# Kernel tuning notes

Hardware: AMD Instinct MI355X
Metric: run time of the kernel (lower is better)

## Reference

```python
import jax, jax.numpy as jnp
import numpy as np

N_NODES = 50000
N_EDGES = 800000
N_GRAPHS = 128


def gcn_conv(x, row, col, W, b, num_nodes):
    # GCNConv: x' = D^-1/2 (A + I) D^-1/2 (x W) + b, with self-loops added.
    h = x @ W  # [N, out]
    # append self-loops
    sl = jnp.arange(num_nodes, dtype=row.dtype)
    r = jnp.concatenate([row, sl])
    c = jnp.concatenate([col, sl])
    deg = jax.ops.segment_sum(jnp.ones_like(r, dtype=h.dtype), r, num_segments=num_nodes)
    dinv = jnp.where(deg > 0, jax.lax.rsqrt(deg), 0.0)
    norm = dinv[r] * dinv[c]  # [E+N]
    msg = h[c] * norm[:, None]  # gather + scale
    out = jax.ops.segment_sum(msg, r, num_segments=num_nodes)
    return out + b


def setup_inputs() -> dict:
    key = jax.random.key(0)
    k = jax.random.split(key, 6)
    x = jax.random.normal(k[0], (N_NODES, 256), dtype=jnp.float32)
    edge_index = jax.random.randint(k[1], (2, N_EDGES), 0, N_NODES, dtype=jnp.int32)
    batch = jnp.sort(jax.random.randint(k[2], (N_NODES,), 0, N_GRAPHS, dtype=jnp.int32))
    W1 = jax.random.normal(k[3], (256, 128), dtype=jnp.float32) * (1.0 / np.sqrt(256))
    b1 = jnp.zeros((128,), dtype=jnp.float32)
    W2 = jax.random.normal(k[4], (128, 32), dtype=jnp.float32) * (1.0 / np.sqrt(128))
    b2 = jnp.zeros((32,), dtype=jnp.float32)
    return {"x": x, "edge_index": edge_index, "batch": batch,
            "W1": W1, "b1": b1, "W2": W2, "b2": b2}


def reference(x, edge_index, batch, W1, b1, W2, b2):
    row, col = edge_index[0], edge_index[1]
    h = gcn_conv(x, row, col, W1, b1, N_NODES)
    h = jax.nn.relu(h)
    # dropout is identity in eval mode (training=False)
    h = gcn_conv(h, row, col, W2, b2, N_NODES)
    # global_mean_pool over batch ids
    sums = jax.ops.segment_sum(h, batch, num_segments=N_GRAPHS)
    cnts = jax.ops.segment_sum(jnp.ones((N_NODES,), dtype=h.dtype), batch, num_segments=N_GRAPHS)
    pooled = sums / jnp.clip(cnts, 1.0)[:, None]  # [G, num_classes]
    return jax.nn.log_softmax(pooled, axis=1)
```

## Files before the change

kernel.cpp:

```cpp
#include <hip/hip_runtime.h>
#include <math.h>

#define N_NODES 50000
#define N_EDGES 800000
#define N_GRAPHS 128
#define DIM0 256
#define DIM1 128
#define DIM2 32

#define NBUCK 196
#define NEB 98

using f32x4 = __attribute__((ext_vector_type(4))) float;
using s16x8 = __attribute__((ext_vector_type(8))) short;

__device__ inline unsigned bf16pack(float a, float b) {
    unsigned ua = __float_as_uint(a), ub = __float_as_uint(b);
    ua = (ua + 0x7fffu + ((ua >> 16) & 1u)) >> 16;
    ub = (ub + 0x7fffu + ((ub >> 16) & 1u)) >> 16;
    return ua | (ub << 16);
}
__device__ inline float2 bf16x2(unsigned p) {
    return make_float2(__uint_as_float(p << 16), __uint_as_float(p & 0xffff0000u));
}

__device__ inline int featOf(int p) {
    return 32 * (p >> 5) + ((p >> 1) & 15) + 16 * (p & 1);
}

__global__ __launch_bounds__(256) void k_preph(const float* __restrict__ W1, uint* __restrict__ W1b,
                                               const float* __restrict__ W2, uint* __restrict__ W2b,
                                               const int* __restrict__ batch, int* gstart,
                                               const int* __restrict__ row, int* __restrict__ hist) {
    __shared__ int h[NBUCK];
    int b = blockIdx.x, t = threadIdx.x;
    if (b < NEB) {
        if (t < NBUCK) h[t] = 0;
        __syncthreads();
#pragma unroll
        for (int i = 0; i < 8; ++i) {
            int idx = b * 2048 + i * 256 + t;
            if (idx < N_EDGES / 4) {
                int4 r4 = ((const int4*)row)[idx];
                atomicAdd(&h[r4.x >> 8], 1);
                atomicAdd(&h[r4.y >> 8], 1);
                atomicAdd(&h[r4.z >> 8], 1);
                atomicAdd(&h[r4.w >> 8], 1);
            }
        }
        __syncthreads();
        if (t < NBUCK) hist[b * NBUCK + t] = h[t];
    } else {
        int g = (b - NEB) * 256 + t;
        {
            int s = g >> 9, tt = (g >> 6) & 7, q = (g >> 4) & 3, n = g & 15;
            int k0 = s * 32 + q * 8;
            int col = tt * 16 + n;
            uint4 o;
            o.x = bf16pack(W1[(size_t)(k0 + 0) * DIM1 + col], W1[(size_t)(k0 + 1) * DIM1 + col]);
            o.y = bf16pack(W1[(size_t)(k0 + 2) * DIM1 + col], W1[(size_t)(k0 + 3) * DIM1 + col]);
            o.z = bf16pack(W1[(size_t)(k0 + 4) * DIM1 + col], W1[(size_t)(k0 + 5) * DIM1 + col]);
            o.w = bf16pack(W1[(size_t)(k0 + 6) * DIM1 + col], W1[(size_t)(k0 + 7) * DIM1 + col]);
            ((uint4*)W1b)[g] = o;
        }
        if (g < 512) {
            int s = g >> 7, tt = (g >> 6) & 1, l = g & 63;
            int n = tt * 16 + (l & 15);
            int kb = s * 32 + (l >> 4) * 8;
            uint4 o;
            o.x = bf16pack(W2[(size_t)featOf(kb + 0) * DIM2 + n], W2[(size_t)featOf(kb + 1) * DIM2 + n]);
            o.y = bf16pack(W2[(size_t)featOf(kb + 2) * DIM2 + n], W2[(size_t)featOf(kb + 3) * DIM2 + n]);
            o.z = bf16pack(W2[(size_t)featOf(kb + 4) * DIM2 + n], W2[(size_t)featOf(kb + 5) * DIM2 + n]);
            o.w = bf16pack(W2[(size_t)featOf(kb + 6) * DIM2 + n], W2[(size_t)featOf(kb + 7) * DIM2 + n]);
            ((uint4*)W2b)[g] = o;
        }
        if (g <= N_GRAPHS) {
            int lo = 0, hi = N_NODES;
            while (lo < hi) { int mid = (lo + hi) >> 1; if (batch[mid] < g) lo = mid + 1; else hi = mid; }
            gstart[g] = lo;
        }
    }
}

__global__ __launch_bounds__(256) void k_place(const int* __restrict__ row, const int* __restrict__ col,
                                               const int* __restrict__ hist, uint* __restrict__ bb,
                                               int* __restrict__ bbase, int* __restrict__ btot) {
    __shared__ int cur[NBUCK];
    __shared__ int tot[NBUCK];
    __shared__ int sc[256];
    int blk = blockIdx.x, t = threadIdx.x;
    int pre = 0, to = 0;
    for (int b2 = 0; b2 < NEB; ++b2) {
        int v = (t < NBUCK) ? hist[b2 * NBUCK + t] : 0;
        to += v;
        if (b2 < blk) pre += v;
    }
    if (t < NBUCK) tot[t] = to;
    sc[t] = (t < NBUCK) ? to : 0;
    __syncthreads();
    for (int off = 1; off < 256; off <<= 1) {
        int x = (t >= off) ? sc[t - off] : 0;
        __syncthreads();
        sc[t] += x;
        __syncthreads();
    }
    if (t < NBUCK) {
        int base = sc[t] - tot[t];
        cur[t] = base + pre;
        if (blk == 0) { bbase[t] = base; btot[t] = tot[t]; }
    }
    __syncthreads();
#pragma unroll
    for (int i = 0; i < 8; ++i) {
        int idx = blk * 2048 + i * 256 + t;
        if (idx < N_EDGES / 4) {
            int4 r4 = ((const int4*)row)[idx];
            int4 c4 = ((const int4*)col)[idx];
            int rs[4] = {r4.x, r4.y, r4.z, r4.w};
            int cs[4] = {c4.x, c4.y, c4.z, c4.w};
#pragma unroll
            for (int j = 0; j < 4; ++j) {
                int pos = atomicAdd(&cur[rs[j] >> 8], 1);
                bb[pos] = ((uint)(rs[j] & 255) << 16) | (uint)cs[j];
            }
        }
    }
}

__global__ __launch_bounds__(256) void k_build(const int* __restrict__ bbase, const int* __restrict__ btot,
                                               const uint* __restrict__ bb,
                                               int* __restrict__ offs, int* __restrict__ cnt,
                                               ushort* __restrict__ csr) {
    __shared__ int c256[256];
    __shared__ int cur256[256];
    __shared__ int wsum[4];
    int b = blockIdx.x, t = threadIdx.x;
    int start = bbase[b];
    int n = btot[b];
    c256[t] = 0;
    __syncthreads();
    for (int i = t; i < n; i += 256) atomicAdd(&c256[bb[start + i] >> 16], 1);
    __syncthreads();
    int w = t >> 6, l = t & 63;
    int v = c256[t];
    int incl = v;
#pragma unroll
    for (int off = 1; off < 64; off <<= 1) {
        int x = __shfl_up(incl, off, 64);
        if (l >= off) incl += x;
    }
    if (l == 63) wsum[w] = incl;
    __syncthreads();
    int woff = 0;
    for (int i = 0; i < w; ++i) woff += wsum[i];
    int excl = incl - v + woff;
    cur256[t] = excl;
    int r = b * 256 + t;
    if (r < N_NODES) { offs[r] = start + excl; cnt[r] = v; }
    __syncthreads();
    for (int i = t; i < n; i += 256) {
        uint e = bb[start + i];
        int pos = atomicAdd(&cur256[e >> 16], 1);
        csr[start + pos] = (ushort)(e & 0xFFFFu);
    }
}

#define G1_BM 128
#define AS_LD 20
__global__ __launch_bounds__(256) void k_gemm1(const float* __restrict__ X, const uint* __restrict__ W1b,
                                               const int* __restrict__ cnt, unsigned* __restrict__ h1u) {
    __shared__ uint w1s[16384];
    __shared__ uint As[G1_BM * AS_LD];
    int t = threadIdx.x;
    int w = t >> 6, lane = t & 63, q = lane >> 4, m16 = lane & 15;
    int rowBase = blockIdx.x * G1_BM;

    {
        const uint4* src = (const uint4*)W1b;
        uint4* dst = (uint4*)w1s;
#pragma unroll
        for (int i = 0; i < 16; ++i) dst[i * 256 + t] = src[i * 256 + t];
    }

    f32x4 acc[2][8];
#pragma unroll
    for (int i = 0; i < 2; ++i)
#pragma unroll
        for (int j = 0; j < 8; ++j) acc[i][j] = (f32x4){0.f, 0.f, 0.f, 0.f};

    int ar = t >> 1, ah = t & 1;
    for (int s = 0; s < 8; ++s) {
        float4 f0 = {0,0,0,0}, f1 = {0,0,0,0}, f2 = {0,0,0,0}, f3 = {0,0,0,0};
        int grow = rowBase + ar;
        if (grow < N_NODES) {
            const float* src = X + (size_t)grow * DIM0 + s * 32 + ah * 16;
            f0 = *(const float4*)(src + 0);
            f1 = *(const float4*)(src + 4);
            f2 = *(const float4*)(src + 8);
            f3 = *(const float4*)(src + 12);
        }
        uint4 p0, p1;
        p0.x = bf16pack(f0.x, f0.y); p0.y = bf16pack(f0.z, f0.w);
        p0.z = bf16pack(f1.x, f1.y); p0.w = bf16pack(f1.z, f1.w);
        p1.x = bf16pack(f2.x, f2.y); p1.y = bf16pack(f2.z, f2.w);
        p1.z = bf16pack(f3.x, f3.y); p1.w = bf16pack(f3.z, f3.w);
        __syncthreads();
        *(uint4*)&As[ar * AS_LD + ah * 8 + 0] = p0;
        *(uint4*)&As[ar * AS_LD + ah * 8 + 4] = p1;
        __syncthreads();

        s16x8 af[2];
#pragma unroll
        for (int rt = 0; rt < 2; ++rt) {
            int arow = w * 32 + rt * 16 + m16;
            af[rt] = *(s16x8*)&As[arow * AS_LD + q * 4];
        }
#pragma unroll
        for (int tt = 0; tt < 8; ++tt) {
            s16x8 bf = *(s16x8*)&w1s[((s * 8 + tt) * 64 + lane) * 4];
            acc[0][tt] = __builtin_amdgcn_mfma_f32_16x16x32_bf16(af[0], bf, acc[0][tt], 0, 0, 0);
            acc[1][tt] = __builtin_amdgcn_mfma_f32_16x16x32_bf16(af[1], bf, acc[1][tt], 0, 0, 0);
        }
    }

#pragma unroll
    for (int rt = 0; rt < 2; ++rt) {
#pragma unroll
        for (int reg = 0; reg < 4; ++reg) {
            int row = rowBase + w * 32 + rt * 16 + q * 4 + reg;
            if (row < N_NODES) {
                float dv = rsqrtf((float)(cnt[row] + 1));
                unsigned* hr = h1u + (size_t)row * 64;
#pragma unroll
                for (int u = 0; u < 4; ++u)
                    hr[u * 16 + m16] = bf16pack(acc[rt][2 * u][reg] * dv, acc[rt][2 * u + 1][reg] * dv);
            }
        }
    }
}

#define A1_LD 68
__global__ __launch_bounds__(256) void k_agg1g2(const unsigned* __restrict__ h1u, const int* __restrict__ cnt,
                                                const int* __restrict__ offs, const ushort* __restrict__ csr,
                                                const float* __restrict__ b1, const uint* __restrict__ W2b,
                                                unsigned* __restrict__ h2u) {
    __shared__ uint a1tile[16 * A1_LD];
    __shared__ float sdi[16];
    int t = threadIdx.x;
    int wv = t >> 6, lane = t & 63;
    int nb16 = blockIdx.x * 16;

#pragma unroll
    for (int i = 0; i < 4; ++i) {
        int m = wv * 4 + i;
        int node = nb16 + m;
        float2 acc = bf16x2(h1u[(size_t)node * 64 + lane]);
        int n = cnt[node];
        const ushort* cp = csr + offs[node];
        int ec = 0;
        if (lane < n) ec = cp[lane];
        int j = 0;
        for (; j + 8 <= n; j += 8) {
            int c0 = __shfl(ec, j),     c1 = __shfl(ec, j + 1), c2 = __shfl(ec, j + 2), c3 = __shfl(ec, j + 3);
            int c4 = __shfl(ec, j + 4), c5 = __shfl(ec, j + 5), c6 = __shfl(ec, j + 6), c7 = __shfl(ec, j + 7);
            unsigned p0 = h1u[(size_t)c0 * 64 + lane];
            unsigned p1 = h1u[(size_t)c1 * 64 + lane];
            unsigned p2 = h1u[(size_t)c2 * 64 + lane];
            unsigned p3 = h1u[(size_t)c3 * 64 + lane];
            unsigned p4 = h1u[(size_t)c4 * 64 + lane];
            unsigned p5 = h1u[(size_t)c5 * 64 + lane];
            unsigned p6 = h1u[(size_t)c6 * 64 + lane];
            unsigned p7 = h1u[(size_t)c7 * 64 + lane];
            float2 v0 = bf16x2(p0), v1 = bf16x2(p1), v2 = bf16x2(p2), v3 = bf16x2(p3);
            float2 v4 = bf16x2(p4), v5 = bf16x2(p5), v6 = bf16x2(p6), v7 = bf16x2(p7);
            acc.x += (v0.x + v1.x) + (v2.x + v3.x) + (v4.x + v5.x) + (v6.x + v7.x);
            acc.y += (v0.y + v1.y) + (v2.y + v3.y) + (v4.y + v5.y) + (v6.y + v7.y);
        }
        for (; j + 4 <= n; j += 4) {
            int c0 = __shfl(ec, j), c1 = __shfl(ec, j + 1), c2 = __shfl(ec, j + 2), c3 = __shfl(ec, j + 3);
            unsigned p0 = h1u[(size_t)c0 * 64 + lane];
            unsigned p1 = h1u[(size_t)c1 * 64 + lane];
            unsigned p2 = h1u[(size_t)c2 * 64 + lane];
            unsigned p3 = h1u[(size_t)c3 * 64 + lane];
            float2 v0 = bf16x2(p0), v1 = bf16x2(p1), v2 = bf16x2(p2), v3 = bf16x2(p3);
            acc.x += (v0.x + v1.x) + (v2.x + v3.x);
            acc.y += (v0.y + v1.y) + (v2.y + v3.y);
        }
        for (; j < n; ++j) {
            int c = __shfl(ec, j);
            float2 v = bf16x2(h1u[(size_t)c * 64 + lane]);
            acc.x += v.x; acc.y += v.y;
        }
        float di = rsqrtf((float)(n + 1));
        if (lane == 0) sdi[m] = di;
        int f0 = (lane >> 4) * 32 + (lane & 15);
        acc.x = fmaxf(acc.x * di + b1[f0], 0.f);
        acc.y = fmaxf(acc.y * di + b1[f0 + 16], 0.f);
        a1tile[m * A1_LD + lane] = bf16pack(acc.x, acc.y);
    }
    __syncthreads();

    if (wv == 0) {
        int q = lane >> 4, m16 = lane & 15;
        f32x4 accA = (f32x4){0.f, 0.f, 0.f, 0.f};
        f32x4 accB = (f32x4){0.f, 0.f, 0.f, 0.f};
#pragma unroll
        for (int s = 0; s < 4; ++s) {
            s16x8 af = *(s16x8*)&a1tile[m16 * A1_LD + s * 16 + q * 4];
            s16x8 bf0 = *(const s16x8*)(W2b + (size_t)((s * 2 + 0) * 64 + lane) * 4);
            s16x8 bf1 = *(const s16x8*)(W2b + (size_t)((s * 2 + 1) * 64 + lane) * 4);
            accA = __builtin_amdgcn_mfma_f32_16x16x32_bf16(af, bf0, accA, 0, 0, 0);
            accB = __builtin_amdgcn_mfma_f32_16x16x32_bf16(af, bf1, accB, 0, 0, 0);
        }
#pragma unroll
        for (int r = 0; r < 4; ++r) {
            int node = nb16 + q * 4 + r;
            float dv = sdi[q * 4 + r];
            h2u[(size_t)node * 16 + m16] = bf16pack(accA[r] * dv, accB[r] * dv);
        }
    }
}

__global__ __launch_bounds__(256) void k_agg2(const unsigned* __restrict__ h2u, const int* __restrict__ cnt,
                                              const int* __restrict__ offs, const ushort* __restrict__ csr,
                                              const float* __restrict__ b2, float* __restrict__ a2) {
    int t = threadIdx.x;
    int node = blockIdx.x * 16 + (t >> 4);
    int l = t & 15;
    float2 acc = bf16x2(h2u[(size_t)node * 16 + l]);
    int n = cnt[node];
    const ushort* cp = csr + offs[node];
    for (int base = 0; base < n; base += 16) {
        int m = min(16, n - base);
        int ec = 0;
        if (l < m) ec = cp[base + l];
        int j = 0;
        for (; j + 4 <= m; j += 4) {
            int c0 = __shfl(ec, j, 16), c1 = __shfl(ec, j + 1, 16);
            int c2 = __shfl(ec, j + 2, 16), c3 = __shfl(ec, j + 3, 16);
            unsigned p0 = h2u[(size_t)c0 * 16 + l];
            unsigned p1 = h2u[(size_t)c1 * 16 + l];
            unsigned p2 = h2u[(size_t)c2 * 16 + l];
            unsigned p3 = h2u[(size_t)c3 * 16 + l];
            float2 v0 = bf16x2(p0), v1 = bf16x2(p1), v2 = bf16x2(p2), v3 = bf16x2(p3);
            acc.x += v0.x + v1.x + v2.x + v3.x;
            acc.y += v0.y + v1.y + v2.y + v3.y;
        }
        for (; j < m; ++j) {
            int c = __shfl(ec, j, 16);
            float2 v = bf16x2(h2u[(size_t)c * 16 + l]);
            acc.x += v.x; acc.y += v.y;
        }
    }
    float di = rsqrtf((float)(n + 1));
    acc.x = acc.x * di + b2[l];
    acc.y = acc.y * di + b2[l + 16];
    ((float2*)a2)[(size_t)node * 16 + l] = acc;
}

__global__ __launch_bounds__(256) void k_pool(const float* __restrict__ a2, const int* __restrict__ gstart,
                                              float* __restrict__ out) {
    __shared__ float sred[8][DIM2];
    int g = blockIdx.x;
    int t = threadIdx.x;
    int s = gstart[g], e = gstart[g + 1];
    int d = t & 31, r = t >> 5;
    float acc = 0.f;
    for (int i = s + r; i < e; i += 8) acc += a2[(size_t)i * DIM2 + d];
    sred[r][d] = acc;
    __syncthreads();
    if (t < DIM2) {
        float sum = 0.f;
#pragma unroll
        for (int j = 0; j < 8; ++j) sum += sred[j][t];
        float cntf = fmaxf((float)(e - s), 1.0f);
        float val = sum / cntf;
        float v = val;
#pragma unroll
        for (int m = 16; m >= 1; m >>= 1) v = fmaxf(v, __shfl_xor(v, m, 32));
        float ex = expf(val - v);
#pragma unroll
        for (int m = 16; m >= 1; m >>= 1) ex += __shfl_xor(ex, m, 32);
        int feat = (t >> 1) + 16 * (t & 1);
        out[g * DIM2 + feat] = val - v - logf(ex);
    }
}

extern "C" void kernel_launch(void* const* d_in, const int* in_sizes, int n_in,
                              void* d_out, int out_size, void* d_ws, size_t ws_size,
                              hipStream_t stream) {
    const float* x     = (const float*)d_in[0];
    const int*   eidx  = (const int*)d_in[1];
    const int*   batch = (const int*)d_in[2];
    const float* W1    = (const float*)d_in[3];
    const float* b1    = (const float*)d_in[4];
    const float* W2    = (const float*)d_in[5];
    const float* b2    = (const float*)d_in[6];
    const int* row = eidx;
    const int* col = eidx + N_EDGES;
    float* out = (float*)d_out;

    char* p = (char*)d_ws;
    int*    cnt    = (int*)p;    p += (size_t)N_NODES * 4;
    int*    offs   = (int*)p;    p += (size_t)N_NODES * 4 + 16;
    int*    gstart = (int*)p;    p += 768;
    uint*   W1b    = (uint*)p;   p += 4096 * 16;
    uint*   W2b    = (uint*)p;   p += 512 * 16;
    int*    hist   = (int*)p;    p += (size_t)NEB * NBUCK * 4 + 32;
    int*    bbase  = (int*)p;    p += 1024;
    int*    btot   = (int*)p;    p += 1024;
    uint*   bb     = (uint*)p;   p += (size_t)N_EDGES * 4;
    ushort* csr    = (ushort*)p; p += (size_t)N_EDGES * 2;
    unsigned* h1u  = (unsigned*)p; p += (size_t)N_NODES * 64 * 4;
    unsigned* h2u  = (unsigned*)p; p += (size_t)N_NODES * 16 * 4;
    float*  a2     = (float*)p;  p += (size_t)N_NODES * DIM2 * 4;

    k_preph<<<NEB + 16, 256, 0, stream>>>(W1, W1b, W2, W2b, batch, gstart, row, hist);
    k_place<<<NEB, 256, 0, stream>>>(row, col, hist, bb, bbase, btot);
    k_build<<<NBUCK, 256, 0, stream>>>(bbase, btot, bb, offs, cnt, csr);

    k_gemm1<<<(N_NODES + G1_BM - 1) / G1_BM, 256, 0, stream>>>(x, W1b, cnt, h1u);
    k_agg1g2<<<N_NODES / 16, 256, 0, stream>>>(h1u, cnt, offs, csr, b1, W2b, h2u);
    k_agg2<<<N_NODES / 16, 256, 0, stream>>>(h2u, cnt, offs, csr, b2, a2);
    k_pool<<<N_GRAPHS, 256, 0, stream>>>(a2, gstart, out);
}
```

Baseline: 204.6 us.

## Merge CSR build into cooperative kernel and fuse agg2 with mean pooling

The three graph-preprocessing kernels (histogram/weight packing, bucket placement, per-bucket CSR build) become one cooperative kernel of 196 blocks separated by grid syncs, which removes two launch gaps. The second aggregation now reduces its 16 nodes per block by graph id and atomically adds into a small pooled buffer, so the a2 intermediate is never written and the separate pooling pass disappears. A tiny final kernel then applies the count division, bias and log_softmax. The costs are grid-sync overhead, float atomics contending on 128 graph rows, and nondeterministic summation order.

```diff
diff --git a/kernel.cpp b/kernel.cpp
--- a/kernel.cpp
+++ b/kernel.cpp
@@ -1,5 +1,8 @@
 #include <hip/hip_runtime.h>
+#include <hip/hip_cooperative_groups.h>
 #include <math.h>
+
+namespace cg = cooperative_groups;
 
 #define N_NODES 50000
 #define N_EDGES 800000
@@ -28,12 +31,24 @@
     return 32 * (p >> 5) + ((p >> 1) & 15) + 16 * (p & 1);
 }
 
-__global__ __launch_bounds__(256) void k_preph(const float* __restrict__ W1, uint* __restrict__ W1b,
-                                               const float* __restrict__ W2, uint* __restrict__ W2b,
-                                               const int* __restrict__ batch, int* gstart,
-                                               const int* __restrict__ row, int* __restrict__ hist) {
+__global__ __launch_bounds__(256) void k_build_coop(const float* __restrict__ W1, uint* __restrict__ W1b,
+                                                    const float* __restrict__ W2, uint* __restrict__ W2b,
+                                                    const int* __restrict__ batch, int* gstart,
+                                                    const int* __restrict__ row, const int* __restrict__ col,
+                                                    int* __restrict__ hist, uint* __restrict__ bb,
+                                                    int* __restrict__ bbase, int* __restrict__ btot,
+                                                    int* __restrict__ offs, int* __restrict__ cnt,
+                                                    ushort* __restrict__ csr, float* __restrict__ pooled) {
     __shared__ int h[NBUCK];
+    __shared__ int cur[NBUCK];
+    __shared__ int tot[NBUCK];
+    __shared__ int sc[256];
+    __shared__ int c256[256];
+    __shared__ int cur256[256];
+    __shared__ int wsum[4];
+    cg::grid_group grid = cg::this_grid();
     int b = blockIdx.x, t = threadIdx.x;
+
     if (b < NEB) {
         if (t < NBUCK) h[t] = 0;
         __syncthreads();
@@ -50,17 +65,17 @@
         }
         __syncthreads();
         if (t < NBUCK) hist[b * NBUCK + t] = h[t];
-    } else {
+    } else if (b < NEB + 16) {
         int g = (b - NEB) * 256 + t;
         {
             int s = g >> 9, tt = (g >> 6) & 7, q = (g >> 4) & 3, n = g & 15;
             int k0 = s * 32 + q * 8;
-            int col = tt * 16 + n;
+            int colw = tt * 16 + n;
             uint4 o;
-            o.x = bf16pack(W1[(size_t)(k0 + 0) * DIM1 + col], W1[(size_t)(k0 + 1) * DIM1 + col]);
-            o.y = bf16pack(W1[(size_t)(k0 + 2) * DIM1 + col], W1[(size_t)(k0 + 3) * DIM1 + col]);
-            o.z = bf16pack(W1[(size_t)(k0 + 4) * DIM1 + col], W1[(size_t)(k0 + 5) * DIM1 + col]);
-            o.w = bf16pack(W1[(size_t)(k0 + 6) * DIM1 + col], W1[(size_t)(k0 + 7) * DIM1 + col]);
+            o.x = bf16pack(W1[(size_t)(k0 + 0) * DIM1 + colw], W1[(size_t)(k0 + 1) * DIM1 + colw]);
+            o.y = bf16pack(W1[(size_t)(k0 + 2) * DIM1 + colw], W1[(size_t)(k0 + 3) * DIM1 + colw]);
+            o.z = bf16pack(W1[(size_t)(k0 + 4) * DIM1 + colw], W1[(size_t)(k0 + 5) * DIM1 + colw]);
+            o.w = bf16pack(W1[(size_t)(k0 + 6) * DIM1 + colw], W1[(size_t)(k0 + 7) * DIM1 + colw]);
             ((uint4*)W1b)[g] = o;
         }
         if (g < 512) {
@@ -79,89 +94,82 @@
             while (lo < hi) { int mid = (lo + hi) >> 1; if (batch[mid] < g) lo = mid + 1; else hi = mid; }
             gstart[g] = lo;
         }
-    }
-}
-
-__global__ __launch_bounds__(256) void k_place(const int* __restrict__ row, const int* __restrict__ col,
-                                               const int* __restrict__ hist, uint* __restrict__ bb,
-                                               int* __restrict__ bbase, int* __restrict__ btot) {
-    __shared__ int cur[NBUCK];
-    __shared__ int tot[NBUCK];
-    __shared__ int sc[256];
-    int blk = blockIdx.x, t = threadIdx.x;
-    int pre = 0, to = 0;
-    for (int b2 = 0; b2 < NEB; ++b2) {
-        int v = (t < NBUCK) ? hist[b2 * NBUCK + t] : 0;
-        to += v;
-        if (b2 < blk) pre += v;
-    }
-    if (t < NBUCK) tot[t] = to;
-    sc[t] = (t < NBUCK) ? to : 0;
-    __syncthreads();
-    for (int off = 1; off < 256; off <<= 1) {
-        int x = (t >= off) ? sc[t - off] : 0;
-        __syncthreads();
-        sc[t] += x;
-        __syncthreads();
-    }
-    if (t < NBUCK) {
-        int base = sc[t] - tot[t];
-        cur[t] = base + pre;
-        if (blk == 0) { bbase[t] = base; btot[t] = tot[t]; }
-    }
-    __syncthreads();
-#pragma unroll
-    for (int i = 0; i < 8; ++i) {
-        int idx = blk * 2048 + i * 256 + t;
-        if (idx < N_EDGES / 4) {
-            int4 r4 = ((const int4*)row)[idx];
-            int4 c4 = ((const int4*)col)[idx];
-            int rs[4] = {r4.x, r4.y, r4.z, r4.w};
-            int cs[4] = {c4.x, c4.y, c4.z, c4.w};
-#pragma unroll
-            for (int j = 0; j < 4; ++j) {
-                int pos = atomicAdd(&cur[rs[j] >> 8], 1);
-                bb[pos] = ((uint)(rs[j] & 255) << 16) | (uint)cs[j];
+    } else if (b == NEB + 16) {
+        for (int i = t; i < N_GRAPHS * DIM2; i += 256) pooled[i] = 0.f;
+    }
+
+    grid.sync();
+
+    if (b < NEB) {
+        int pre = 0, to = 0;
+        for (int b2 = 0; b2 < NEB; ++b2) {
+            int v = (t < NBUCK) ? hist[b2 * NBUCK + t] : 0;
+            to += v;
+            if (b2 < b) pre += v;
+        }
+        if (t < NBUCK) tot[t] = to;
+        sc[t] = (t < NBUCK) ? to : 0;
+        __syncthreads();
+        for (int off = 1; off < 256; off <<= 1) {
+            int x = (t >= off) ? sc[t - off] : 0;
+            __syncthreads();
+            sc[t] += x;
+            __syncthreads();
+        }
+        if (t < NBUCK) {
+            int base = sc[t] - tot[t];
+            cur[t] = base + pre;
+            if (b == 0) { bbase[t] = base; btot[t] = tot[t]; }
+        }
+        __syncthreads();
+#pragma unroll
+        for (int i = 0; i < 8; ++i) {
+            int idx = b * 2048 + i * 256 + t;
+            if (idx < N_EDGES / 4) {
+                int4 r4 = ((const int4*)row)[idx];
+                int4 c4 = ((const int4*)col)[idx];
+                int rs[4] = {r4.x, r4.y, r4.z, r4.w};
+                int cs[4] = {c4.x, c4.y, c4.z, c4.w};
+#pragma unroll
+                for (int j = 0; j < 4; ++j) {
+                    int pos = atomicAdd(&cur[rs[j] >> 8], 1);
+                    bb[pos] = ((uint)(rs[j] & 255) << 16) | (uint)cs[j];
+                }
             }
         }
     }
-}
-
-__global__ __launch_bounds__(256) void k_build(const int* __restrict__ bbase, const int* __restrict__ btot,
-                                               const uint* __restrict__ bb,
-                                               int* __restrict__ offs, int* __restrict__ cnt,
-                                               ushort* __restrict__ csr) {
-    __shared__ int c256[256];
-    __shared__ int cur256[256];
-    __shared__ int wsum[4];
-    int b = blockIdx.x, t = threadIdx.x;
-    int start = bbase[b];
-    int n = btot[b];
-    c256[t] = 0;
-    __syncthreads();
-    for (int i = t; i < n; i += 256) atomicAdd(&c256[bb[start + i] >> 16], 1);
-    __syncthreads();
-    int w = t >> 6, l = t & 63;
-    int v = c256[t];
-    int incl = v;
-#pragma unroll
-    for (int off = 1; off < 64; off <<= 1) {
-        int x = __shfl_up(incl, off, 64);
-        if (l >= off) incl += x;
-    }
-    if (l == 63) wsum[w] = incl;
-    __syncthreads();
-    int woff = 0;
-    for (int i = 0; i < w; ++i) woff += wsum[i];
-    int excl = incl - v + woff;
-    cur256[t] = excl;
-    int r = b * 256 + t;
-    if (r < N_NODES) { offs[r] = start + excl; cnt[r] = v; }
-    __syncthreads();
-    for (int i = t; i < n; i += 256) {
-        uint e = bb[start + i];
-        int pos = atomicAdd(&cur256[e >> 16], 1);
-        csr[start + pos] = (ushort)(e & 0xFFFFu);
+
+    grid.sync();
+
+    {
+        int start = bbase[b];
+        int n = btot[b];
+        c256[t] = 0;
+        __syncthreads();
+        for (int i = t; i < n; i += 256) atomicAdd(&c256[bb[start + i] >> 16], 1);
+        __syncthreads();
+        int w = t >> 6, l = t & 63;
+        int v = c256[t];
+        int incl = v;
+#pragma unroll
+        for (int off = 1; off < 64; off <<= 1) {
+            int x = __shfl_up(incl, off, 64);
+            if (l >= off) incl += x;
+        }
+        if (l == 63) wsum[w] = incl;
+        __syncthreads();
+        int woff = 0;
+        for (int i = 0; i < w; ++i) woff += wsum[i];
+        int excl = incl - v + woff;
+        cur256[t] = excl;
+        int r = b * 256 + t;
+        if (r < N_NODES) { offs[r] = start + excl; cnt[r] = v; }
+        __syncthreads();
+        for (int i = t; i < n; i += 256) {
+            uint e = bb[start + i];
+            int pos = atomicAdd(&cur256[e >> 16], 1);
+            csr[start + pos] = (ushort)(e & 0xFFFFu);
+        }
     }
 }
 
@@ -321,11 +329,13 @@
     }
 }
 
-__global__ __launch_bounds__(256) void k_agg2(const unsigned* __restrict__ h2u, const int* __restrict__ cnt,
-                                              const int* __restrict__ offs, const ushort* __restrict__ csr,
-                                              const float* __restrict__ b2, float* __restrict__ a2) {
+__global__ __launch_bounds__(256) void k_agg2pool(const unsigned* __restrict__ h2u, const int* __restrict__ cnt,
+                                                  const int* __restrict__ offs, const ushort* __restrict__ csr,
+                                                  const int* __restrict__ batch, float* __restrict__ pooled) {
+    __shared__ float2 red[16][16];
     int t = threadIdx.x;
-    int node = blockIdx.x * 16 + (t >> 4);
+    int nb16 = blockIdx.x * 16;
+    int node = nb16 + (t >> 4);
     int l = t & 15;
     float2 acc = bf16x2(h2u[(size_t)node * 16 + l]);
     int n = cnt[node];
@@ -353,37 +363,43 @@
         }
     }
     float di = rsqrtf((float)(n + 1));
-    acc.x = acc.x * di + b2[l];
-    acc.y = acc.y * di + b2[l + 16];
-    ((float2*)a2)[(size_t)node * 16 + l] = acc;
-}
-
-__global__ __launch_bounds__(256) void k_pool(const float* __restrict__ a2, const int* __restrict__ gstart,
-                                              float* __restrict__ out) {
-    __shared__ float sred[8][DIM2];
+    red[t >> 4][l] = make_float2(acc.x * di, acc.y * di);
+    __syncthreads();
+    if (t < 16) {
+        float2 run = make_float2(0.f, 0.f);
+        int gprev = batch[nb16];
+        for (int m = 0; m < 16; ++m) {
+            int g = batch[nb16 + m];
+            if (g != gprev) {
+                atomicAdd(&pooled[gprev * DIM2 + t], run.x);
+                atomicAdd(&pooled[gprev * DIM2 + t + 16], run.y);
+                run = make_float2(0.f, 0.f);
+                gprev = g;
+            }
+            float2 v = red[m][t];
+            run.x += v.x; run.y += v.y;
+        }
+        atomicAdd(&pooled[gprev * DIM2 + t], run.x);
+        atomicAdd(&pooled[gprev * DIM2 + t + 16], run.y);
+    }
+}
+
+__global__ __launch_bounds__(64) void k_final(const float* __restrict__ pooled, const int* __restrict__ gstart,
+                                              const float* __restrict__ b2, float* __restrict__ out) {
     int g = blockIdx.x;
-    int t = threadIdx.x;
-    int s = gstart[g], e = gstart[g + 1];
-    int d = t & 31, r = t >> 5;
-    float acc = 0.f;
-    for (int i = s + r; i < e; i += 8) acc += a2[(size_t)i * DIM2 + d];
-    sred[r][d] = acc;
-    __syncthreads();
-    if (t < DIM2) {
-        float sum = 0.f;
-#pragma unroll
-        for (int j = 0; j < 8; ++j) sum += sred[j][t];
-        float cntf = fmaxf((float)(e - s), 1.0f);
-        float val = sum / cntf;
-        float v = val;
-#pragma unroll
-        for (int m = 16; m >= 1; m >>= 1) v = fmaxf(v, __shfl_xor(v, m, 32));
-        float ex = expf(val - v);
-#pragma unroll
-        for (int m = 16; m >= 1; m >>= 1) ex += __shfl_xor(ex, m, 32);
-        int feat = (t >> 1) + 16 * (t & 1);
-        out[g * DIM2 + feat] = val - v - logf(ex);
-    }
+    int lane = threadIdx.x;
+    float cntf = fmaxf((float)(gstart[g + 1] - gstart[g]), 1.0f);
+    float val = 0.f, v = -INFINITY;
+    if (lane < DIM2) {
+        val = pooled[g * DIM2 + lane] / cntf + b2[lane];
+        v = val;
+    }
+#pragma unroll
+    for (int m = 16; m >= 1; m >>= 1) v = fmaxf(v, __shfl_xor(v, m, 32));
+    float ex = (lane < DIM2) ? expf(val - v) : 0.f;
+#pragma unroll
+    for (int m = 16; m >= 1; m >>= 1) ex += __shfl_xor(ex, m, 32);
+    if (lane < DIM2) out[g * DIM2 + lane] = val - v - logf(ex);
 }
 
 extern "C" void kernel_launch(void* const* d_in, const int* in_sizes, int n_in,
@@ -409,18 +425,23 @@
     int*    hist   = (int*)p;    p += (size_t)NEB * NBUCK * 4 + 32;
     int*    bbase  = (int*)p;    p += 1024;
     int*    btot   = (int*)p;    p += 1024;
+    float*  pooled = (float*)p;  p += (size_t)N_GRAPHS * DIM2 * 4;
     uint*   bb     = (uint*)p;   p += (size_t)N_EDGES * 4;
     ushort* csr    = (ushort*)p; p += (size_t)N_EDGES * 2;
     unsigned* h1u  = (unsigned*)p; p += (size_t)N_NODES * 64 * 4;
     unsigned* h2u  = (unsigned*)p; p += (size_t)N_NODES * 16 * 4;
-    float*  a2     = (float*)p;  p += (size_t)N_NODES * DIM2 * 4;
-
-    k_preph<<<NEB + 16, 256, 0, stream>>>(W1, W1b, W2, W2b, batch, gstart, row, hist);
-    k_place<<<NEB, 256, 0, stream>>>(row, col, hist, bb, bbase, btot);
-    k_build<<<NBUCK, 256, 0, stream>>>(bbase, btot, bb, offs, cnt, csr);
+
+    {
+        void* args[] = { (void*)&W1, (void*)&W1b, (void*)&W2, (void*)&W2b,
+                         (void*)&batch, (void*)&gstart, (void*)&row, (void*)&col,
+                         (void*)&hist, (void*)&bb, (void*)&bbase, (void*)&btot,
+                         (void*)&offs, (void*)&cnt, (void*)&csr, (void*)&pooled };
+        hipLaunchCooperativeKernel((const void*)k_build_coop, dim3(NBUCK), dim3(256),
+                                   args, 0, stream);
+    }
 
     k_gemm1<<<(N_NODES + G1_BM - 1) / G1_BM, 256, 0, stream>>>(x, W1b, cnt, h1u);
     k_agg1g2<<<N_NODES / 16, 256, 0, stream>>>(h1u, cnt, offs, csr, b1, W2b, h2u);
-    k_agg2<<<N_NODES / 16, 256, 0, stream>>>(h2u, cnt, offs, csr, b2, a2);
-    k_pool<<<N_GRAPHS, 256, 0, stream>>>(a2, gstart, out);
-}
+    k_agg2pool<<<N_NODES / 16, 256, 0, stream>>>(h2u, cnt, offs, csr, batch, pooled);
+    k_final<<<N_GRAPHS, 64, 0, stream>>>(pooled, gstart, b2, out);
+}
```

Result: slower. 257.2 us (+25.7%).
